# Kernel optimization log

Hardware: AMD Instinct MI355X
Metric: run time of the kernel (lower is better)

## Reference

```python
import math
import jax, jax.numpy as jnp
import numpy as np
from jax import lax

# FPN anchor layout: 1024x768 image, strides {4,8,16,32,64}, 3 anchors/location
NUM_PER_LEVEL = (147456, 36864, 9216, 2304, 576)
A_TOTAL = sum(NUM_PER_LEVEL)
BATCH = 8
PRE_NMS_TOP_N = 1000   # testing
POST_NMS_TOP_N = 1000  # testing
NMS_THRESH = 0.7
SCORE_THRESH = 0.0
MIN_SIZE = 1.0
IMG_H, IMG_W = 768.0, 1024.0
BBOX_XFORM_CLIP = math.log(1000.0 / 16.0)


def setup_inputs() -> dict:
    key = jax.random.key(0)
    k1, k2, k3, k4, k5, k6 = jax.random.split(key, 6)
    objectness = jax.random.normal(k1, (BATCH, A_TOTAL), jnp.float32)
    pred_bbox_deltas = jax.random.normal(k2, (BATCH, A_TOTAL, 4), jnp.float32) * 0.2
    # valid anchor boxes (x1, y1, x2, y2)
    cx = jax.random.uniform(k3, (A_TOTAL,), jnp.float32) * IMG_W
    cy = jax.random.uniform(k4, (A_TOTAL,), jnp.float32) * IMG_H
    w = 16.0 + jax.random.uniform(k5, (A_TOTAL,), jnp.float32) * 176.0
    h = 16.0 + jax.random.uniform(k6, (A_TOTAL,), jnp.float32) * 176.0
    anchors = jnp.stack([cx - 0.5 * w, cy - 0.5 * h, cx + 0.5 * w, cy + 0.5 * h], -1)
    return {"objectness": objectness, "pred_bbox_deltas": pred_bbox_deltas, "anchors": anchors}


def _nms_image(boxes, scores, lvl, valid):
    """batched_nms (level-offset trick) + post-NMS top-k, fixed shapes.
    boxes [K,4], scores [K], lvl [K] int, valid [K] bool -> [POST_NMS_TOP_N, 5]"""
    K = boxes.shape[0]
    s = jnp.where(valid, scores, -1.0)
    order = jnp.argsort(-s)  # decreasing score (invalid last)
    b = boxes[order]
    s = s[order]
    v = valid[order]
    # offset boxes per level so cross-level boxes never overlap (torchvision batched_nms)
    offset = lvl[order].astype(b.dtype) * (jnp.max(lax.stop_gradient(boxes)) + 1.0)
    nb = lax.stop_gradient(b) + offset[:, None]
    area = (nb[:, 2] - nb[:, 0]) * (nb[:, 3] - nb[:, 1])
    lt = jnp.maximum(nb[:, None, :2], nb[None, :, :2])  # [K,K,2]
    rb = jnp.minimum(nb[:, None, 2:], nb[None, :, 2:])
    wh = jnp.clip(rb - lt, 0.0)
    inter = wh[..., 0] * wh[..., 1]
    iou = inter / jnp.maximum(area[:, None] + area[None, :] - inter, 1e-9)
    pos = jnp.arange(K)

    def body(keep, i):
        sup = keep[i] & (iou[i] > NMS_THRESH) & (pos > i)
        return keep & ~sup, None

    keep, _ = lax.scan(body, v, pos)
    masked = jnp.where(keep, s, -1.0)
    top_s, top_i = lax.top_k(masked, POST_NMS_TOP_N)  # kept, decreasing score
    sel_b = b[top_i]
    ok = top_s > -0.5
    sel_b = jnp.where(ok[:, None], sel_b, 0.0)
    top_s = jnp.where(ok, top_s, 0.0)
    return jnp.concatenate([sel_b, top_s[:, None]], axis=-1)


def reference(objectness, pred_bbox_deltas, anchors):
    # --- box decode (BoxCoder, weights (1,1,1,1)) ---
    wa = anchors[:, 2] - anchors[:, 0]
    ha = anchors[:, 3] - anchors[:, 1]
    cxa = anchors[:, 0] + 0.5 * wa
    cya = anchors[:, 1] + 0.5 * ha
    dx, dy = pred_bbox_deltas[..., 0], pred_bbox_deltas[..., 1]
    dw = jnp.minimum(pred_bbox_deltas[..., 2], BBOX_XFORM_CLIP)
    dh = jnp.minimum(pred_bbox_deltas[..., 3], BBOX_XFORM_CLIP)
    pcx = dx * wa + cxa
    pcy = dy * ha + cya
    pw = jnp.exp(dw) * wa
    ph = jnp.exp(dh) * ha
    proposals = jnp.stack(
        [pcx - 0.5 * pw, pcy - 0.5 * ph, pcx + 0.5 * pw, pcy + 0.5 * ph], axis=-1
    )  # [B, A, 4]

    # --- per-level pre-NMS top-k (_get_top_n_idx) ---
    levels = jnp.concatenate(
        [jnp.full((n,), i, jnp.int32) for i, n in enumerate(NUM_PER_LEVEL)]
    )
    idx_parts = []
    off = 0
    for n in NUM_PER_LEVEL:
        k = min(PRE_NMS_TOP_N, n)
        _, ti = lax.top_k(objectness[:, off:off + n], k)
        idx_parts.append(ti + off)
        off += n
    top_idx = jnp.concatenate(idx_parts, axis=1)  # [B, K]

    scores = jax.nn.sigmoid(jnp.take_along_axis(objectness, top_idx, axis=1))
    lvl = levels[top_idx]
    boxes = jnp.take_along_axis(proposals, top_idx[..., None], axis=1)  # [B,K,4]

    # --- clip to image ---
    x1 = jnp.clip(boxes[..., 0], 0.0, IMG_W)
    y1 = jnp.clip(boxes[..., 1], 0.0, IMG_H)
    x2 = jnp.clip(boxes[..., 2], 0.0, IMG_W)
    y2 = jnp.clip(boxes[..., 3], 0.0, IMG_H)
    boxes = jnp.stack([x1, y1, x2, y2], axis=-1)

    # remove_small_boxes + score threshold (as validity mask; fixed shapes)
    valid = ((x2 - x1) >= MIN_SIZE) & ((y2 - y1) >= MIN_SIZE) & (scores >= SCORE_THRESH)

    # --- per-image batched NMS + post-NMS top-k ---
    return jax.vmap(_nms_image)(boxes, scores, lvl, valid)  # [B, POST_NMS_TOP_N, 5]
```

## Files before the change

kernel.cpp:

```cpp
#include <hip/hip_runtime.h>
#include <math.h>

#pragma clang fp contract(off)

#define A_TOTAL 196416
#define BATCH 8
#define KTOT 4576
#define NLEV 5
#define MSPLIT 16
#define RCAP 6144

static __device__ const int d_aoff[NLEV] = {0, 147456, 184320, 193536, 195840};
static __device__ const int d_n[NLEV]    = {147456, 36864, 9216, 2304, 576};
static __device__ const int d_k[NLEV]    = {1000, 1000, 1000, 1000, 576};
static __device__ const int d_spl[NLEV]  = {8, 2, 1, 1, 1};
static __device__ const int d_bp[NLEV]   = {0, 8, 10, 11, 12};
static __device__ const int d_pb_l[13]    = {0,0,0,0,0,0,0,0,1,1,2,3,4};
static __device__ const int d_pb_part[13] = {0,1,2,3,4,5,6,7,0,1,0,0,0};

#define TM_IOU (0.699999988079071044921875 + 0x1p-25)

__device__ inline unsigned int mono(float f) {
  unsigned int u = __float_as_uint(f);
  return (u & 0x80000000u) ? ~u : (u | 0x80000000u);
}
__device__ inline float imono(unsigned int m) {
  return __uint_as_float((m & 0x80000000u) ? (m & 0x7FFFFFFFu) : ~m);
}

__device__ inline int cnt_gt(const float* A, int n, float s) {
  int lo = 0, hi = n;
  while (lo < hi) { int mid = (lo + hi) >> 1; if (A[mid] > s) lo = mid + 1; else hi = mid; }
  return lo;
}
__device__ inline int cnt_ge(const float* A, int n, float s) {
  int lo = 0, hi = n;
  while (lo < hi) { int mid = (lo + hi) >> 1; if (A[mid] >= s) lo = mid + 1; else hi = mid; }
  return lo;
}

__global__ __launch_bounds__(1024) void k_hist(const float* __restrict__ obj,
                                               int* __restrict__ hist_g,
                                               int* __restrict__ cnt_g,
                                               float* __restrict__ maxblk) {
  int blk = blockIdx.x;
  int tid = threadIdx.x;
  if (blk == 0) {
    for (int i = tid; i < 640; i += 1024) maxblk[i] = 0.0f;
    for (int i = tid; i < 40; i += 1024) cnt_g[i] = 0;
  }
  int b = blk / 13, pb = blk % 13;
  int l = d_pb_l[pb], part = d_pb_part[pb];
  int slice = d_n[l] / d_spl[l];
  int start = d_aoff[l] + part * slice;
  const float4* p4 = (const float4*)(obj + (size_t)b * A_TOTAL + start);
  int s4 = slice >> 2;
  __shared__ int h[4096];
  for (int i = tid; i < 4096; i += 1024) h[i] = 0;
  __syncthreads();
  for (int i = tid; i < s4; i += 1024) {
    float4 v = p4[i];
    atomicAdd(&h[mono(v.x) >> 20], 1);
    atomicAdd(&h[mono(v.y) >> 20], 1);
    atomicAdd(&h[mono(v.z) >> 20], 1);
    atomicAdd(&h[mono(v.w) >> 20], 1);
  }
  __syncthreads();
  int* outp = hist_g + (size_t)blk * 4096;
  for (int i = tid; i < 4096; i += 1024) outp[i] = h[i];
}

__global__ __launch_bounds__(1024) void k_collect(const float* __restrict__ obj,
                                                  const int* __restrict__ hist_g,
                                                  int* __restrict__ cnt_g,
                                                  unsigned long long* __restrict__ cand_g) {
  int blk = blockIdx.x;
  int b = blk / 13, pb = blk % 13;
  int l = d_pb_l[pb], part = d_pb_part[pb];
  int bl = b * NLEV + l;
  const int k = d_k[l];
  int tid = threadIdx.x;
  __shared__ int t[4096];
  __shared__ int grp[256];
  __shared__ unsigned int sP;
  __shared__ __align__(16) unsigned long long lbuf[RCAP];
  __shared__ int s_cnt, s_base;
  int parts = d_spl[l];
  const int* hb = hist_g + (size_t)(b * 13 + d_bp[l]) * 4096;
  for (int bin = tid; bin < 4096; bin += 1024) {
    int s = 0;
    for (int p = 0; p < parts; ++p) s += hb[p * 4096 + bin];
    t[bin] = s;
  }
  if (tid == 0) s_cnt = 0;
  __syncthreads();
  if (tid < 256) {
    int s = 0;
    for (int j = 0; j < 16; ++j) s += t[tid * 16 + j];
    grp[tid] = s;
  }
  __syncthreads();
  if (tid == 0) {
    int cum = 0, g, d;
    for (g = 255; g >= 0; --g) {
      if (cum + grp[g] >= k) break;
      cum += grp[g];
    }
    for (d = 15; d >= 0; --d) {
      int c = t[g * 16 + d];
      if (cum + c >= k) break;
      cum += c;
    }
    sP = (unsigned int)(g * 16 + d);
  }
  __syncthreads();
  unsigned int P = sP;
  int slice = d_n[l] / parts;
  int start = d_aoff[l] + part * slice;
  const float4* p4 = (const float4*)(obj + (size_t)b * A_TOTAL + start);
  int s4 = slice >> 2;
  int lbase = part * slice;
  for (int i = tid; i < s4; i += 1024) {
    float4 v = p4[i];
    unsigned int a[4] = {mono(v.x), mono(v.y), mono(v.z), mono(v.w)};
#pragma unroll
    for (int c = 0; c < 4; ++c) {
      if ((a[c] >> 20) >= P) {
        int slot = atomicAdd(&s_cnt, 1);
        if (slot < RCAP) {
          int idx = lbase + 4 * i + c;
          lbuf[slot] = ((unsigned long long)a[c] << 32) |
                       (unsigned int)(~(unsigned int)idx);
        }
      }
    }
  }
  __syncthreads();
  int cnt = min(s_cnt, RCAP);
  if (tid == 0) s_base = atomicAdd(&cnt_g[bl], cnt);
  __syncthreads();
  int base = s_base;
  for (int i = tid; i < cnt; i += 1024) {
    int slot = base + i;
    if (slot < RCAP) cand_g[(size_t)bl * RCAP + slot] = lbuf[i];
  }
}

__global__ __launch_bounds__(256) void k_rankdec(const unsigned long long* __restrict__ cand_g,
                                                 const int* __restrict__ cnt_g,
                                                 const float* __restrict__ deltas,
                                                 const float* __restrict__ anchors,
                                                 float* __restrict__ sc0,
                                                 float4* __restrict__ box0,
                                                 float* __restrict__ maxblk) {
  int bl = blockIdx.x >> 4, part = blockIdx.x & 15;
  int b = bl / NLEV, l = bl % NLEV;
  const int k = d_k[l], aoff = d_aoff[l];
  int cnt = min(cnt_g[bl], RCAP);
  if (part * 256 >= cnt) return;
  __shared__ __align__(16) unsigned long long cb[RCAP];
  __shared__ unsigned int s_max;
  int tid = threadIdx.x;
  if (tid == 0) s_max = 0u;
  const unsigned long long* src = cand_g + (size_t)bl * RCAP;
  for (int i = tid; i < cnt; i += 256) cb[i] = src[i];
  __syncthreads();
  int myi = part * 256 + tid;
  float mx = 0.0f;
  if (myi < cnt) {
    unsigned long long e = cb[myi];
    int rank = 0;
    int nc2 = cnt >> 1;
    const ulonglong2* c2 = (const ulonglong2*)cb;
    for (int j = 0; j < nc2; ++j) {
      ulonglong2 v = c2[j];
      rank += (v.x > e) + (v.y > e);
    }
    if (cnt & 1) rank += (cb[cnt - 1] > e);
    if (rank < k) {
      unsigned int key = (unsigned int)(e >> 32);
      unsigned int idx = ~(unsigned int)(e & 0xFFFFFFFFull);
      float o = imono(key);
      int gidx = aoff + (int)idx;
      const float* dl = deltas + ((size_t)b * A_TOTAL + gidx) * 4;
      const float* an = anchors + (size_t)gidx * 4;
      float a0 = an[0], a1 = an[1], a2 = an[2], a3 = an[3];
      float wa = a2 - a0, ha = a3 - a1;
      float cxa = a0 + 0.5f * wa, cya = a1 + 0.5f * ha;
      float dx = dl[0], dy = dl[1];
      const float CLIPV = 4.135166556742356f;
      float dw = fminf(dl[2], CLIPV), dh = fminf(dl[3], CLIPV);
      float pcx = dx * wa + cxa;
      float pcy = dy * ha + cya;
      float pw = (float)exp((double)dw) * wa;
      float ph = (float)exp((double)dh) * ha;
      float x1 = pcx - 0.5f * pw, y1 = pcy - 0.5f * ph;
      float x2 = pcx + 0.5f * pw, y2 = pcy + 0.5f * ph;
      x1 = fminf(fmaxf(x1, 0.0f), 1024.0f);
      x2 = fminf(fmaxf(x2, 0.0f), 1024.0f);
      y1 = fminf(fmaxf(y1, 0.0f), 768.0f);
      y2 = fminf(fmaxf(y2, 0.0f), 768.0f);
      float s = (float)(1.0 / (1.0 + exp(-(double)o)));
      bool valid = ((x2 - x1) >= 1.0f) && ((y2 - y1) >= 1.0f) && (s >= 0.0f);
      sc0[bl * 1024 + rank] = valid ? s : -1.0f;
      box0[bl * 1024 + rank] = make_float4(x1, y1, x2, y2);
      mx = fmaxf(fmaxf(x1, y1), fmaxf(x2, y2));
    }
  }
  atomicMax(&s_max, __float_as_uint(mx));
  __syncthreads();
  if (tid == 0) maxblk[blockIdx.x] = __uint_as_float(s_max);
}

__global__ __launch_bounds__(1024) void k_compact(const float* __restrict__ sc0,
                                                  const float4* __restrict__ box0,
                                                  const float* __restrict__ maxblk,
                                                  float* __restrict__ lvlsc,
                                                  float4* __restrict__ lvlraw,
                                                  float4* __restrict__ lvlofs,
                                                  int* __restrict__ g_V) {
  int bl = blockIdx.x;
  int b = bl / NLEV, l = bl % NLEV;
  const int k = d_k[l];
  int tid = threadIdx.x, lane = tid & 63, wv = tid >> 6;
  __shared__ float s_mv;
  __shared__ int s_wcnt[16];
  if (wv == 0) {
    float v = (lane < 80) ? maxblk[b * 80 + lane] : 0.0f;
    float v2 = (lane + 64 < 80) ? maxblk[b * 80 + lane + 64] : 0.0f;
    v = fmaxf(v, v2);
#pragma unroll
    for (int s = 1; s < 64; s <<= 1) v = fmaxf(v, __shfl_xor(v, s));
    if (lane == 0) s_mv = v;
  }
  bool in = tid < k;
  float s = in ? sc0[bl * 1024 + tid] : -1.0f;
  bool valid = in && (s >= 0.0f);
  unsigned long long mb = __ballot(valid);
  if (lane == 0) s_wcnt[wv] = __popcll(mb);
  __syncthreads();
  int pre = 0;
  for (int w = 0; w < wv; ++w) pre += s_wcnt[w];
  int j = pre + __popcll(mb & ((1ull << lane) - 1ull));
  float off = (float)l * (s_mv + 1.0f);
  if (valid) {
    lvlsc[bl * 1024 + j] = s;
    float4 bx = box0[bl * 1024 + tid];
    lvlraw[bl * 1024 + j] = bx;
    lvlofs[bl * 1024 + j] = make_float4(bx.x + off, bx.y + off, bx.z + off, bx.w + off);
  }
  if (tid == 0) {
    int t = 0;
    for (int w = 0; w < 16; ++w) t += s_wcnt[w];
    g_V[bl] = t;
  }
}

__global__ __launch_bounds__(1024) void k_mask(const float4* __restrict__ lvlofs,
                                               const int* __restrict__ g_V,
                                               unsigned long long* __restrict__ masks) {
  int blk = blockIdx.x;
  int bl = blk / MSPLIT, part = blk % MSPLIT;
  int V = g_V[bl];
  int row0 = part * 64;
  if (row0 >= V) return;
  int tid = threadIdx.x, lane = tid & 63, w = tid >> 6;
  __shared__ float4 lbox[1024];
  for (int i = tid; i < V; i += 1024) lbox[i] = lvlofs[bl * 1024 + i];
  __syncthreads();
  int i = row0 + lane;
  if (i >= V) return;
  float4 bb = lbox[i];
  float ba = (bb.z - bb.x) * (bb.w - bb.y);
  unsigned long long bits = 0ull;
  int jbase = w * 64;
  if (jbase + 63 > i && jbase < V) {
    int jhi = min(64, V - jbase);
    for (int jo = 0; jo < jhi; ++jo) {
      int j = jbase + jo;
      float4 cb = lbox[j];
      float ca = (cb.z - cb.x) * (cb.w - cb.y);
      float xx1 = fmaxf(bb.x, cb.x), yy1 = fmaxf(bb.y, cb.y);
      float xx2 = fminf(bb.z, cb.z), yy2 = fminf(bb.w, cb.w);
      float wd = fmaxf(xx2 - xx1, 0.0f), ht = fmaxf(yy2 - yy1, 0.0f);
      float inter = wd * ht;
      float denom = fmaxf(ba + ca - inter, 1e-9f);
      if ((j > i) && ((double)inter >= TM_IOU * (double)denom)) bits |= (1ull << jo);
    }
  }
  masks[((size_t)bl * 16 + w) * 1024 + i] = bits;
}

__global__ __launch_bounds__(1024) void k_scan(const unsigned long long* __restrict__ masks,
                                               const int* __restrict__ g_V,
                                               unsigned long long* __restrict__ keepbits) {
  int bl = blockIdx.x;
  int tid = threadIdx.x, lane = tid & 63, w = tid >> 6;
  int V = g_V[bl];
  const int nch = (V + 63) / 64;
  const unsigned long long* M = masks + (size_t)bl * 16 * 1024;
  __shared__ unsigned long long s_remv[16];
  __shared__ unsigned long long s_D[2][72];
  __shared__ unsigned long long s_dw;
  if (tid < 16) s_remv[tid] = ~0ull;
  int base_w = w * 64;
  unsigned long long init_w;
  if (V <= base_w) init_w = ~0ull;
  else if (V >= base_w + 64) init_w = 0ull;
  else init_w = (~0ull) << (V - base_w);
  if (w == 0 && nch > 0) s_D[0][lane] = (lane < V) ? M[lane] : 0ull;
  if (tid < 8) { s_D[0][64 + tid] = 0ull; s_D[1][64 + tid] = 0ull; }
  unsigned long long acc = 0ull;
  __syncthreads();

  for (int c = 0; c < nch; ++c) {
    unsigned long long val = 0ull;
    int r = 64 * c + lane;
    if (w > c && w < nch && r < V) val = M[(size_t)w * 1024 + r];
    if (w == c) {
      unsigned long long red = acc;
#pragma unroll
      for (int s = 1; s < 64; s <<= 1) red |= __shfl_xor(red, s);
      unsigned long long dw = init_w | red;
      const unsigned long long* D = s_D[c & 1];
      unsigned long long pb[8];
#pragma unroll
      for (int u = 0; u < 8; ++u) pb[u] = D[u];
#pragma unroll
      for (int g = 0; g < 8; ++g) {
#pragma unroll
        for (int u = 0; u < 8; ++u) {
          int j = g * 8 + u;
          if (!((dw >> j) & 1ull)) dw |= pb[u];
          pb[u] = D[j + 8];
        }
      }
      if (lane == 0) { s_dw = dw; s_remv[c] = dw; }
    }
    if (w == c + 1 && w < nch) {
      int rr = 64 * (c + 1) + lane;
      s_D[(c + 1) & 1][lane] = (rr < V) ? M[(size_t)(c + 1) * 1024 + rr] : 0ull;
    }
    __syncthreads();
    if (w > c && w < nch) {
      unsigned long long kept = ~s_dw;
      if ((kept >> lane) & 1ull) acc |= val;
    }
    __syncthreads();
  }
  if (tid < 16) keepbits[bl * 16 + tid] = ~s_remv[tid];
}

__global__ __launch_bounds__(1024) void k_out(const float* __restrict__ lvlsc,
                                              const float4* __restrict__ lvlraw,
                                              const unsigned long long* __restrict__ keepbits,
                                              const int* __restrict__ g_V,
                                              float* __restrict__ out) {
  int b = blockIdx.x;
  int tid = threadIdx.x, lane = tid & 63, wv = tid >> 6;
  __shared__ float ksc[NLEV * 1024];
  __shared__ int kj[NLEV * 1024];
  __shared__ int sK[NLEV];
  __shared__ int s_wcnt[16];
  for (int i = tid; i < 5000; i += 1024) out[(size_t)b * 5000 + i] = 0.0f;
  for (int l = 0; l < NLEV; ++l) {
    int bl = b * NLEV + l;
    int V = g_V[bl];
    bool kept = (tid < V) && ((keepbits[bl * 16 + (tid >> 6)] >> (tid & 63)) & 1ull);
    unsigned long long mb = __ballot(kept);
    if (lane == 0) s_wcnt[wv] = __popcll(mb);
    __syncthreads();
    int pre = 0;
    for (int w = 0; w < wv; ++w) pre += s_wcnt[w];
    int r = pre + __popcll(mb & ((1ull << lane) - 1ull));
    if (kept) { ksc[l * 1024 + r] = lvlsc[bl * 1024 + tid]; kj[l * 1024 + r] = tid; }
    if (tid == 0) {
      int t = 0;
      for (int w = 0; w < 16; ++w) t += s_wcnt[w];
      sK[l] = t;
    }
    __syncthreads();
  }
  int K[NLEV];
  for (int l = 0; l < NLEV; ++l) K[l] = sK[l];
  for (int l = 0; l < NLEV; ++l) {
    if (tid < K[l]) {
      float s = ksc[l * 1024 + tid];
      int rank = tid;
      for (int l2 = 0; l2 < NLEV; ++l2) {
        if (l2 == l) continue;
        const float* A = ksc + l2 * 1024;
        rank += (l2 < l) ? cnt_ge(A, K[l2], s) : cnt_gt(A, K[l2], s);
      }
      if (rank < 1000) {
        float4 bx = lvlraw[(size_t)(b * NLEV + l) * 1024 + kj[l * 1024 + tid]];
        float* op = out + (size_t)b * 5000 + (size_t)rank * 5;
        op[0] = bx.x; op[1] = bx.y; op[2] = bx.z; op[3] = bx.w; op[4] = s;
      }
    }
  }
}

extern "C" void kernel_launch(void* const* d_in, const int* in_sizes, int n_in,
                              void* d_out, int out_size, void* d_ws, size_t ws_size,
                              hipStream_t stream) {
  const float* obj     = (const float*)d_in[0];
  const float* deltas  = (const float*)d_in[1];
  const float* anchors = (const float*)d_in[2];
  float* out = (float*)d_out;

  char* p = (char*)d_ws;
  float4* box0   = (float4*)p; p += (size_t)40 * 1024 * sizeof(float4);
  float4* lvlraw = (float4*)p; p += (size_t)40 * 1024 * sizeof(float4);
  float4* lvlofs = (float4*)p; p += (size_t)40 * 1024 * sizeof(float4);
  unsigned long long* cand_g   = (unsigned long long*)p; p += (size_t)40 * RCAP * 8;
  unsigned long long* masks    = (unsigned long long*)p; p += (size_t)40 * 16 * 1024 * 8;
  unsigned long long* keepbits = (unsigned long long*)p; p += (size_t)40 * 16 * 8;
  int*   hist_g = (int*)p;   p += (size_t)104 * 4096 * 4;
  int*   cnt_g  = (int*)p;   p += 40 * 4;
  float* maxblk = (float*)p; p += 640 * 4;
  float* sc0    = (float*)p; p += (size_t)40 * 1024 * 4;
  float* lvlsc  = (float*)p; p += (size_t)40 * 1024 * 4;
  int*   g_V    = (int*)p;   p += 40 * 4;

  hipLaunchKernelGGL(k_hist, dim3(BATCH * 13), dim3(1024), 0, stream,
                     obj, hist_g, cnt_g, maxblk);
  hipLaunchKernelGGL(k_collect, dim3(BATCH * 13), dim3(1024), 0, stream,
                     obj, hist_g, cnt_g, cand_g);
  hipLaunchKernelGGL(k_rankdec, dim3(BATCH * NLEV * 16), dim3(256), 0, stream,
                     cand_g, cnt_g, deltas, anchors, sc0, box0, maxblk);
  hipLaunchKernelGGL(k_compact, dim3(BATCH * NLEV), dim3(1024), 0, stream,
                     sc0, box0, maxblk, lvlsc, lvlraw, lvlofs, g_V);
  hipLaunchKernelGGL(k_mask, dim3(BATCH * NLEV * MSPLIT), dim3(1024), 0, stream,
                     lvlofs, g_V, masks);
  hipLaunchKernelGGL(k_scan, dim3(BATCH * NLEV), dim3(1024), 0, stream,
                     masks, g_V, keepbits);
  hipLaunchKernelGGL(k_out, dim3(BATCH), dim3(1024), 0, stream,
                     lvlsc, lvlraw, keepbits, g_V, out);
}
```

Before: 211.2 us.

## Fuse compaction into IoU mask kernel and rank candidates on 32-bit keys

The separate compaction kernel is folded into the mask kernel. Each of the 16 mask blocks per image-level now redoes the valid-box compaction and builds the offset boxes directly in shared memory, so the lvlofs buffer and one launch go away. The rank kernel now keeps only the 32-bit score keys in shared memory and counts greater and equal keys with 128-bit loads. Ties fall back to comparing the full 64-bit entries from global memory. The cost is compaction work repeated 16 times per image-level and a slow fallback path when keys tie.

Measured after the change: 317.9 us. 1.51x slower.

```diff
diff --git a/kernel.cpp b/kernel.cpp
--- a/kernel.cpp
+++ b/kernel.cpp
@@ -158,29 +158,43 @@
   const int k = d_k[l], aoff = d_aoff[l];
   int cnt = min(cnt_g[bl], RCAP);
   if (part * 256 >= cnt) return;
-  __shared__ __align__(16) unsigned long long cb[RCAP];
+  __shared__ __align__(16) unsigned int cb[RCAP];
   __shared__ unsigned int s_max;
   int tid = threadIdx.x;
   if (tid == 0) s_max = 0u;
   const unsigned long long* src = cand_g + (size_t)bl * RCAP;
-  for (int i = tid; i < cnt; i += 256) cb[i] = src[i];
+  for (int i = tid; i < cnt; i += 256) cb[i] = (unsigned int)(src[i] >> 32);
   __syncthreads();
   int myi = part * 256 + tid;
   float mx = 0.0f;
   if (myi < cnt) {
-    unsigned long long e = cb[myi];
-    int rank = 0;
-    int nc2 = cnt >> 1;
-    const ulonglong2* c2 = (const ulonglong2*)cb;
-    for (int j = 0; j < nc2; ++j) {
-      ulonglong2 v = c2[j];
-      rank += (v.x > e) + (v.y > e);
-    }
-    if (cnt & 1) rank += (cb[cnt - 1] > e);
+    unsigned long long e = src[myi];
+    unsigned int k32 = (unsigned int)(e >> 32);
+    int gt = 0, eq = 0;
+    int nc4 = cnt >> 2;
+    const uint4* c4 = (const uint4*)cb;
+    for (int j = 0; j < nc4; ++j) {
+      uint4 v = c4[j];
+      gt += (v.x > k32) + (v.y > k32) + (v.z > k32) + (v.w > k32);
+      eq += (v.x == k32) + (v.y == k32) + (v.z == k32) + (v.w == k32);
+    }
+    for (int j = nc4 << 2; j < cnt; ++j) {
+      unsigned int v = cb[j];
+      gt += (v > k32);
+      eq += (v == k32);
+    }
+    int rank = gt;
+    if (eq > 1) {
+      for (int j = 0; j < cnt; ++j) {
+        if (cb[j] == k32 && j != myi) {
+          unsigned long long f = src[j];
+          rank += (f > e) ? 1 : 0;
+        }
+      }
+    }
     if (rank < k) {
-      unsigned int key = (unsigned int)(e >> 32);
       unsigned int idx = ~(unsigned int)(e & 0xFFFFFFFFull);
-      float o = imono(key);
+      float o = imono(k32);
       int gidx = aoff + (int)idx;
       const float* dl = deltas + ((size_t)b * A_TOTAL + gidx) * 4;
       const float* an = anchors + (size_t)gidx * 4;
@@ -212,20 +226,22 @@
   if (tid == 0) maxblk[blockIdx.x] = __uint_as_float(s_max);
 }
 
-__global__ __launch_bounds__(1024) void k_compact(const float* __restrict__ sc0,
-                                                  const float4* __restrict__ box0,
-                                                  const float* __restrict__ maxblk,
-                                                  float* __restrict__ lvlsc,
-                                                  float4* __restrict__ lvlraw,
-                                                  float4* __restrict__ lvlofs,
-                                                  int* __restrict__ g_V) {
-  int bl = blockIdx.x;
+__global__ __launch_bounds__(1024) void k_mask(const float* __restrict__ sc0,
+                                               const float4* __restrict__ box0,
+                                               const float* __restrict__ maxblk,
+                                               float* __restrict__ lvlsc,
+                                               float4* __restrict__ lvlraw,
+                                               int* __restrict__ g_V,
+                                               unsigned long long* __restrict__ masks) {
+  int blk = blockIdx.x;
+  int bl = blk / MSPLIT, part = blk % MSPLIT;
   int b = bl / NLEV, l = bl % NLEV;
   const int k = d_k[l];
-  int tid = threadIdx.x, lane = tid & 63, wv = tid >> 6;
+  int tid = threadIdx.x, lane = tid & 63, w = tid >> 6;
+  __shared__ float4 lbox[1024];
   __shared__ float s_mv;
   __shared__ int s_wcnt[16];
-  if (wv == 0) {
+  if (w == 0) {
     float v = (lane < 80) ? maxblk[b * 80 + lane] : 0.0f;
     float v2 = (lane + 64 < 80) ? maxblk[b * 80 + lane + 64] : 0.0f;
     v = fmaxf(v, v2);
@@ -237,37 +253,26 @@
   float s = in ? sc0[bl * 1024 + tid] : -1.0f;
   bool valid = in && (s >= 0.0f);
   unsigned long long mb = __ballot(valid);
-  if (lane == 0) s_wcnt[wv] = __popcll(mb);
+  if (lane == 0) s_wcnt[w] = __popcll(mb);
   __syncthreads();
   int pre = 0;
-  for (int w = 0; w < wv; ++w) pre += s_wcnt[w];
+  for (int ww = 0; ww < w; ++ww) pre += s_wcnt[ww];
   int j = pre + __popcll(mb & ((1ull << lane) - 1ull));
+  int V = 0;
+  for (int ww = 0; ww < 16; ++ww) V += s_wcnt[ww];
   float off = (float)l * (s_mv + 1.0f);
   if (valid) {
-    lvlsc[bl * 1024 + j] = s;
     float4 bx = box0[bl * 1024 + tid];
-    lvlraw[bl * 1024 + j] = bx;
-    lvlofs[bl * 1024 + j] = make_float4(bx.x + off, bx.y + off, bx.z + off, bx.w + off);
-  }
-  if (tid == 0) {
-    int t = 0;
-    for (int w = 0; w < 16; ++w) t += s_wcnt[w];
-    g_V[bl] = t;
-  }
-}
-
-__global__ __launch_bounds__(1024) void k_mask(const float4* __restrict__ lvlofs,
-                                               const int* __restrict__ g_V,
-                                               unsigned long long* __restrict__ masks) {
-  int blk = blockIdx.x;
-  int bl = blk / MSPLIT, part = blk % MSPLIT;
-  int V = g_V[bl];
+    lbox[j] = make_float4(bx.x + off, bx.y + off, bx.z + off, bx.w + off);
+    if (part == 0) {
+      lvlsc[bl * 1024 + j] = s;
+      lvlraw[bl * 1024 + j] = bx;
+    }
+  }
+  if (part == 0 && tid == 0) g_V[bl] = V;
+  __syncthreads();
   int row0 = part * 64;
   if (row0 >= V) return;
-  int tid = threadIdx.x, lane = tid & 63, w = tid >> 6;
-  __shared__ float4 lbox[1024];
-  for (int i = tid; i < V; i += 1024) lbox[i] = lvlofs[bl * 1024 + i];
-  __syncthreads();
   int i = row0 + lane;
   if (i >= V) return;
   float4 bb = lbox[i];
@@ -277,15 +282,15 @@
   if (jbase + 63 > i && jbase < V) {
     int jhi = min(64, V - jbase);
     for (int jo = 0; jo < jhi; ++jo) {
-      int j = jbase + jo;
-      float4 cb = lbox[j];
+      int jj = jbase + jo;
+      float4 cb = lbox[jj];
       float ca = (cb.z - cb.x) * (cb.w - cb.y);
       float xx1 = fmaxf(bb.x, cb.x), yy1 = fmaxf(bb.y, cb.y);
       float xx2 = fminf(bb.z, cb.z), yy2 = fminf(bb.w, cb.w);
       float wd = fmaxf(xx2 - xx1, 0.0f), ht = fmaxf(yy2 - yy1, 0.0f);
       float inter = wd * ht;
       float denom = fmaxf(ba + ca - inter, 1e-9f);
-      if ((j > i) && ((double)inter >= TM_IOU * (double)denom)) bits |= (1ull << jo);
+      if ((jj > i) && ((double)inter >= TM_IOU * (double)denom)) bits |= (1ull << jo);
     }
   }
   masks[((size_t)bl * 16 + w) * 1024 + i] = bits;
@@ -330,9 +335,9 @@
       for (int g = 0; g < 8; ++g) {
 #pragma unroll
         for (int u = 0; u < 8; ++u) {
-          int j = g * 8 + u;
-          if (!((dw >> j) & 1ull)) dw |= pb[u];
-          pb[u] = D[j + 8];
+          int jj = g * 8 + u;
+          if (!((dw >> jj) & 1ull)) dw |= pb[u];
+          pb[u] = D[jj + 8];
         }
       }
       if (lane == 0) { s_dw = dw; s_remv[c] = dw; }
@@ -412,7 +417,6 @@
   char* p = (char*)d_ws;
   float4* box0   = (float4*)p; p += (size_t)40 * 1024 * sizeof(float4);
   float4* lvlraw = (float4*)p; p += (size_t)40 * 1024 * sizeof(float4);
-  float4* lvlofs = (float4*)p; p += (size_t)40 * 1024 * sizeof(float4);
   unsigned long long* cand_g   = (unsigned long long*)p; p += (size_t)40 * RCAP * 8;
   unsigned long long* masks    = (unsigned long long*)p; p += (size_t)40 * 16 * 1024 * 8;
   unsigned long long* keepbits = (unsigned long long*)p; p += (size_t)40 * 16 * 8;
@@ -429,10 +433,8 @@
                      obj, hist_g, cnt_g, cand_g);
   hipLaunchKernelGGL(k_rankdec, dim3(BATCH * NLEV * 16), dim3(256), 0, stream,
                      cand_g, cnt_g, deltas, anchors, sc0, box0, maxblk);
-  hipLaunchKernelGGL(k_compact, dim3(BATCH * NLEV), dim3(1024), 0, stream,
-                     sc0, box0, maxblk, lvlsc, lvlraw, lvlofs, g_V);
   hipLaunchKernelGGL(k_mask, dim3(BATCH * NLEV * MSPLIT), dim3(1024), 0, stream,
-                     lvlofs, g_V, masks);
+                     sc0, box0, maxblk, lvlsc, lvlraw, g_V, masks);
   hipLaunchKernelGGL(k_scan, dim3(BATCH * NLEV), dim3(1024), 0, stream,
                      masks, g_V, keepbits);
   hipLaunchKernelGGL(k_out, dim3(BATCH), dim3(1024), 0, stream,
```
